# Kernel optimization log

Hardware: AMD Instinct MI355X
Metric: run time of the kernel (lower is better)

The kernel has to match this reference:

```python
import jax, jax.numpy as jnp
import numpy as np

N_NODES = 50000
N_EDGES = 1600000
IN_DIM = 128
HID = 128
SHARED = 64
N_GRAPHS = 2048


def setup_inputs() -> dict:
    key = jax.random.key(0)
    ks = jax.random.split(key, 16)
    x = jax.random.normal(ks[0], (N_NODES, IN_DIM), dtype=jnp.float32)
    edge_index = jax.random.randint(ks[1], (2, N_EDGES), 0, N_NODES, dtype=jnp.int64)
    batch = jnp.sort(jax.random.randint(ks[2], (N_NODES,), 0, N_GRAPHS, dtype=jnp.int64))

    def lin(k, fan_in, fan_out):
        bound = 1.0 / np.sqrt(fan_in)
        kw, kb = jax.random.split(k)
        W = jax.random.uniform(kw, (fan_in, fan_out), minval=-bound, maxval=bound, dtype=jnp.float32)
        b = jax.random.uniform(kb, (fan_out,), minval=-bound, maxval=bound, dtype=jnp.float32)
        return W, b

    W1a, b1a = lin(ks[3], IN_DIM, HID)
    W1b, b1b = lin(ks[4], HID, HID)
    W2a, b2a = lin(ks[5], HID, HID)
    W2b, b2b = lin(ks[6], HID, HID)
    Ws, bs = lin(ks[7], HID, SHARED)
    WlS, blS = lin(ks[8], SHARED, 1)
    WlP, blP = lin(ks[9], SHARED, 1)
    WnR, bnR = lin(ks[10], SHARED, 1)
    return dict(x=x, edge_index=edge_index, batch=batch,
                W1a=W1a, b1a=b1a, W1b=W1b, b1b=b1b,
                W2a=W2a, b2a=b2a, W2b=W2b, b2b=b2b,
                Ws=Ws, bs=bs, WlS=WlS, blS=blS, WlP=WlP, blP=blP, WnR=WnR, bnR=bnR)


def gin_conv(x, src, dst, Wa, ba, Wb, bb):
    # GINConv (eps=0): h_i = MLP(x_i + sum_{j->i} x_j)
    agg = jax.ops.segment_sum(x[src], dst, num_segments=N_NODES)
    h = x + agg
    h = jax.nn.relu(h @ Wa + ba)
    return h @ Wb + bb


def reference(x, edge_index, batch, W1a, b1a, W1b, b1b, W2a, b2a, W2b, b2b,
              Ws, bs, WlS, blS, WlP, blP, WnR, bnR):
    src, dst = edge_index[0], edge_index[1]
    h = jax.nn.relu(gin_conv(x, src, dst, W1a, b1a, W1b, b1b))
    h = jax.nn.relu(gin_conv(h, src, dst, W2a, b2a, W2b, b2b))
    # global mean pool over graph ids
    sums = jax.ops.segment_sum(h, batch, num_segments=N_GRAPHS)
    counts = jax.ops.segment_sum(jnp.ones((h.shape[0],), h.dtype), batch, num_segments=N_GRAPHS)
    pooled = sums / jnp.maximum(counts, 1.0)[:, None]
    g = jax.nn.relu(pooled @ Ws + bs)
    out_logS = (g @ WlS + blS)[:, 0]
    out_logP = (g @ WlP + blP)[:, 0]
    out_NR = (g @ WnR + bnR)[:, 0]
    return (out_logS, out_logP, out_NR)
```

## Files before the change

### kernel.cpp

```cpp
#include <hip/hip_runtime.h>
#include <hip/hip_bf16.h>


#define IN_DIM 128
#define NFINE 256
#define BIN_EPB 4096
#define SRCCH 16
#define NSLOT 3200
#define SPT 7

typedef float  f32x4  __attribute__((ext_vector_type(4)));
typedef short  bf16x4 __attribute__((ext_vector_type(4)));
typedef short  bf16x8 __attribute__((ext_vector_type(8)));

__device__ __forceinline__ unsigned short bf16_rne(float v) {
    unsigned u = __float_as_uint(v);
    unsigned t = u + 0x7fffu + ((u >> 16) & 1u);
    return (unsigned short)(t >> 16);
}


__global__ __launch_bounds__(256) void setup_kernel(
    const float4* __restrict__ xin, uint4* __restrict__ xb, int n8,
    const float* __restrict__ W0, const float* __restrict__ W1,
    const float* __restrict__ W2, const float* __restrict__ W3,
    unsigned short* __restrict__ Wh, unsigned short* __restrict__ Wl,
    int* __restrict__ bcur, float* __restrict__ pooled, int npool)
{
    int gid = blockIdx.x * 256 + threadIdx.x;
    if (gid < n8) {
        float4 a = xin[gid * 2];
        float4 b = xin[gid * 2 + 1];
        float v[8] = {a.x, a.y, a.z, a.w, b.x, b.y, b.z, b.w};
        unsigned r[4];
#pragma unroll
        for (int j = 0; j < 4; ++j)
            r[j] = (unsigned)bf16_rne(v[j * 2]) | ((unsigned)bf16_rne(v[j * 2 + 1]) << 16);
        xb[gid] = make_uint4(r[0], r[1], r[2], r[3]);
    }
    if (gid < 4 * 16384) {
        int m   = gid >> 14;
        int idx = gid & 16383;
        const float* W = (m == 0) ? W0 : (m == 1) ? W1 : (m == 2) ? W2 : W3;
        int k = idx >> 7, n = idx & 127;
        float v = W[idx];
        unsigned short hh = bf16_rne(v);
        float hf = __uint_as_float(((unsigned)hh) << 16);
        unsigned short ll = bf16_rne(v - hf);
        Wh[m * 16384 + n * 128 + k] = hh;
        Wl[m * 16384 + n * 128 + k] = ll;
    }
    if (gid < NFINE) bcur[gid] = 0;
    if (gid < npool) pooled[gid] = 0.f;
}


__global__ __launch_bounds__(256) void bin_kernel(
    const int* __restrict__ src, const int* __restrict__ dst,
    int2* __restrict__ buckets, int* __restrict__ bcur,
    int n_edges, int n_nodes, int cap)
{
    __shared__ int cnt[NFINE];
    __shared__ int base[NFINE];
    for (int i = threadIdx.x; i < NFINE; i += 256) cnt[i] = 0;
    __syncthreads();

    const int e0 = blockIdx.x * BIN_EPB + threadIdx.x * 16;
    int ne = n_edges - e0;
    if (ne < 0) ne = 0;
    if (ne > 16) ne = 16;

    int d[16], s[16], off[16];
    if (ne == 16) {
#pragma unroll
        for (int q = 0; q < 4; ++q) {
            int4 dv = *(const int4*)(dst + e0 + q * 4);
            int4 sv = *(const int4*)(src + e0 + q * 4);
            d[q * 4 + 0] = dv.x; d[q * 4 + 1] = dv.y;
            d[q * 4 + 2] = dv.z; d[q * 4 + 3] = dv.w;
            s[q * 4 + 0] = sv.x; s[q * 4 + 1] = sv.y;
            s[q * 4 + 2] = sv.z; s[q * 4 + 3] = sv.w;
        }
    } else {
#pragma unroll
        for (int j = 0; j < 16; ++j) {
            d[j] = (j < ne) ? dst[e0 + j] : 0;
            s[j] = (j < ne) ? src[e0 + j] : 0;
        }
    }
#pragma unroll
    for (int j = 0; j < 16; ++j)
        if (j < ne) {
            int b = (int)(((long long)d[j] * NFINE) / n_nodes);
            off[j] = atomicAdd(&cnt[b], 1);
        }
    __syncthreads();
    for (int i = threadIdx.x; i < NFINE; i += 256)
        base[i] = atomicAdd(&bcur[i], cnt[i]);
    __syncthreads();
#pragma unroll
    for (int j = 0; j < 16; ++j)
        if (j < ne) {
            int b = (int)(((long long)d[j] * NFINE) / n_nodes);
            buckets[(size_t)b * cap + base[b] + off[j]] = make_int2(d[j], s[j]);
        }
}

__global__ __launch_bounds__(512) void csr_fused_kernel(
    const int2* __restrict__ buckets, const int* __restrict__ bcnt,
    int* __restrict__ row_start, int* __restrict__ csr_src,
    int cap, int n_nodes, int n_edges)
{
    __shared__ int bc[NFINE];
    __shared__ int h[NSLOT];
    __shared__ int tsum[512];
    __shared__ int bbase_s;

    const int b = blockIdx.x;
    const int t = threadIdx.x;
    const int lo_n = (int)(((long long)b * n_nodes + NFINE - 1) / NFINE);
    const int hi_n = (int)(((long long)(b + 1) * n_nodes + NFINE - 1) / NFINE);
    const int sl = hi_n - lo_n;

    for (int i = t; i < NFINE; i += 512) bc[i] = bcnt[i];
    for (int i = t; i < NSLOT; i += 512) h[i] = 0;
    __syncthreads();
    if (t == 0) {
        int s = 0;
        for (int i = 0; i < b; ++i) s += bc[i];
        bbase_s = s;
    }
    const int nb = bc[b];
    const int2* bp = buckets + (size_t)b * cap;
    __syncthreads();

    for (int i = t; i < nb; i += 512) {
        int2 e = bp[i];
        int key = (e.x - lo_n) * SRCCH + (int)(((long long)e.y * SRCCH) / n_nodes);
        atomicAdd(&h[key], 1);
    }
    __syncthreads();

    int base = 0;
#pragma unroll
    for (int j = 0; j < SPT; ++j) {
        int slot = t * SPT + j;
        if (slot < NSLOT) {
            int v = h[slot];
            h[slot] = base;
            base += v;
        }
    }
    tsum[t] = base;
    __syncthreads();
    for (int off = 1; off < 512; off <<= 1) {
        int tmp = (t >= off) ? tsum[t - off] : 0;
        __syncthreads();
        tsum[t] += tmp;
        __syncthreads();
    }
    int texcl = tsum[t] - base + bbase_s;
#pragma unroll
    for (int j = 0; j < SPT; ++j) {
        int slot = t * SPT + j;
        if (slot < NSLOT) h[slot] += texcl;
    }
    __syncthreads();
    for (int i = t; i < sl; i += 512) row_start[lo_n + i] = h[i * SRCCH];
    if (b == NFINE - 1 && t == 0) row_start[n_nodes] = n_edges;
    __syncthreads();

    for (int i = t; i < nb; i += 512) {
        int2 e = bp[i];
        int key = (e.x - lo_n) * SRCCH + (int)(((long long)e.y * SRCCH) / n_nodes);
        csr_src[atomicAdd(&h[key], 1)] = e.y;
    }
}

#define HSTRIDE 132

__device__ __forceinline__ void add_row8(float acc[8], uint4 r) {
    union { unsigned u; float f; } c;
    c.u = r.x << 16;         acc[0] += c.f;
    c.u = r.x & 0xffff0000u; acc[1] += c.f;
    c.u = r.y << 16;         acc[2] += c.f;
    c.u = r.y & 0xffff0000u; acc[3] += c.f;
    c.u = r.z << 16;         acc[4] += c.f;
    c.u = r.z & 0xffff0000u; acc[5] += c.f;
    c.u = r.w << 16;         acc[6] += c.f;
    c.u = r.w & 0xffff0000u; acc[7] += c.f;
}

template <int LAYER>
__global__ __launch_bounds__(512) void fused_gin_layer_kernel(
    const float* __restrict__ xf,
    const uint4* __restrict__ selfh,
    const uint4* __restrict__ selfl,
    const uint4* __restrict__ nbr,
    const int* __restrict__ row_start, const int* __restrict__ csr_src,
    const unsigned short* __restrict__ Wa_h, const unsigned short* __restrict__ Wa_l,
    const float* __restrict__ ba,
    const unsigned short* __restrict__ Wb_h, const unsigned short* __restrict__ Wb_l,
    const float* __restrict__ bb,
    unsigned short* __restrict__ Ch, unsigned short* __restrict__ Cl,
    float* __restrict__ pooled, const int* __restrict__ batch, int M)
{
    __shared__ __align__(16) unsigned short LDSBUF[2][64][HSTRIDE];
    __shared__ int sbatch[64];
    auto& Hh = LDSBUF[0];
    auto& Hl = LDSBUF[1];

    const int t    = threadIdx.x;
    const int brow = blockIdx.x * 64;

    {
        const int lane = t & 15;
        const int gr   = t >> 4;
#pragma unroll
        for (int it = 0; it < 2; ++it) {
            const int rl   = it * 32 + gr;
            const int node = brow + rl;
            float acc[8] = {0.f, 0.f, 0.f, 0.f, 0.f, 0.f, 0.f, 0.f};
            if (node < M) {
                if constexpr (LAYER == 1) {
                    const f32x4* xfr = (const f32x4*)(xf + (size_t)node * IN_DIM + lane * 8);
                    f32x4 a0 = xfr[0];
                    f32x4 a1 = xfr[1];
                    acc[0] = a0.x; acc[1] = a0.y; acc[2] = a0.z; acc[3] = a0.w;
                    acc[4] = a1.x; acc[5] = a1.y; acc[6] = a1.z; acc[7] = a1.w;
                } else {
                    add_row8(acc, selfh[(size_t)node * 16 + lane]);
                    add_row8(acc, selfl[(size_t)node * 16 + lane]);
                }
                const int lo = row_start[node];
                const int hi = row_start[node + 1];
                int e = lo;
                for (; e + 3 < hi; e += 4) {
                    int s0 = csr_src[e];
                    int s1 = csr_src[e + 1];
                    int s2 = csr_src[e + 2];
                    int s3 = csr_src[e + 3];
                    uint4 r0 = nbr[(size_t)s0 * 16 + lane];
                    uint4 r1 = nbr[(size_t)s1 * 16 + lane];
                    uint4 r2 = nbr[(size_t)s2 * 16 + lane];
                    uint4 r3 = nbr[(size_t)s3 * 16 + lane];
                    add_row8(acc, r0);
                    add_row8(acc, r1);
                    add_row8(acc, r2);
                    add_row8(acc, r3);
                }
                for (; e < hi; ++e)
                    add_row8(acc, nbr[(size_t)csr_src[e] * 16 + lane]);
            }
            unsigned short hh[8], ll[8];
#pragma unroll
            for (int j = 0; j < 8; ++j) {
                unsigned short h = bf16_rne(acc[j]);
                hh[j] = h;
                ll[j] = bf16_rne(acc[j] - __uint_as_float(((unsigned)h) << 16));
            }
            *(bf16x4*)&Hh[rl][lane * 8]     = *(const bf16x4*)&hh[0];
            *(bf16x4*)&Hh[rl][lane * 8 + 4] = *(const bf16x4*)&hh[4];
            *(bf16x4*)&Hl[rl][lane * 8]     = *(const bf16x4*)&ll[0];
            *(bf16x4*)&Hl[rl][lane * 8 + 4] = *(const bf16x4*)&ll[4];
        }
    }
    __syncthreads();

    const int wave = t >> 6;
    const int lane = t & 63;
    const int l15  = lane & 15;
    const int quad = lane >> 4;
    const int rh   = (wave & 1) * 32;
    const int cq   = (wave >> 1) * 32;

    f32x4 acc[2][2];
#pragma unroll
    for (int ti = 0; ti < 2; ++ti)
#pragma unroll
        for (int ct = 0; ct < 2; ++ct) acc[ti][ct] = {0.f, 0.f, 0.f, 0.f};

#pragma unroll
    for (int k0 = 0; k0 < IN_DIM; k0 += 32) {
        const int hk = k0 + quad * 8;
        bf16x8 ah[2], al[2];
#pragma unroll
        for (int ti = 0; ti < 2; ++ti) {
            const int hr = rh + ti * 16 + l15;
            bf16x4 h0 = *(const bf16x4*)&Hh[hr][hk];
            bf16x4 h1 = *(const bf16x4*)&Hh[hr][hk + 4];
            bf16x4 l0 = *(const bf16x4*)&Hl[hr][hk];
            bf16x4 l1 = *(const bf16x4*)&Hl[hr][hk + 4];
            ah[ti] = __builtin_shufflevector(h0, h1, 0, 1, 2, 3, 4, 5, 6, 7);
            al[ti] = __builtin_shufflevector(l0, l1, 0, 1, 2, 3, 4, 5, 6, 7);
        }
#pragma unroll
        for (int ct = 0; ct < 2; ++ct) {
            const size_t woff = (size_t)(cq + ct * 16 + l15) * IN_DIM + k0 + quad * 8;
            bf16x8 wh = *(const bf16x8*)(Wa_h + woff);
            bf16x8 wl = *(const bf16x8*)(Wa_l + woff);
            acc[0][ct] = __builtin_amdgcn_mfma_f32_16x16x32_bf16(ah[0], wh, acc[0][ct], 0, 0, 0);
            acc[1][ct] = __builtin_amdgcn_mfma_f32_16x16x32_bf16(ah[1], wh, acc[1][ct], 0, 0, 0);
            acc[0][ct] = __builtin_amdgcn_mfma_f32_16x16x32_bf16(al[0], wh, acc[0][ct], 0, 0, 0);
            acc[1][ct] = __builtin_amdgcn_mfma_f32_16x16x32_bf16(al[1], wh, acc[1][ct], 0, 0, 0);
            acc[0][ct] = __builtin_amdgcn_mfma_f32_16x16x32_bf16(ah[0], wl, acc[0][ct], 0, 0, 0);
            acc[1][ct] = __builtin_amdgcn_mfma_f32_16x16x32_bf16(ah[1], wl, acc[1][ct], 0, 0, 0);
        }
    }
    __syncthreads();

#pragma unroll
    for (int ti = 0; ti < 2; ++ti) {
#pragma unroll
        for (int ct = 0; ct < 2; ++ct) {
            int col = cq + ct * 16 + l15;
            float b = ba[col];
#pragma unroll
            for (int r = 0; r < 4; ++r) {
                int rl = rh + ti * 16 + quad * 4 + r;
                float v = fmaxf(acc[ti][ct][r] + b, 0.f);
                unsigned short hh = bf16_rne(v);
                Hh[rl][col] = hh;
                Hl[rl][col] = bf16_rne(v - __uint_as_float(((unsigned)hh) << 16));
            }
            acc[ti][ct] = {0.f, 0.f, 0.f, 0.f};
        }
    }
    __syncthreads();

#pragma unroll
    for (int k0 = 0; k0 < IN_DIM; k0 += 32) {
        const int hk = k0 + quad * 8;
        bf16x8 ah[2], al[2];
#pragma unroll
        for (int ti = 0; ti < 2; ++ti) {
            const int hr = rh + ti * 16 + l15;
            bf16x4 h0 = *(const bf16x4*)&Hh[hr][hk];
            bf16x4 h1 = *(const bf16x4*)&Hh[hr][hk + 4];
            bf16x4 l0 = *(const bf16x4*)&Hl[hr][hk];
            bf16x4 l1 = *(const bf16x4*)&Hl[hr][hk + 4];
            ah[ti] = __builtin_shufflevector(h0, h1, 0, 1, 2, 3, 4, 5, 6, 7);
            al[ti] = __builtin_shufflevector(l0, l1, 0, 1, 2, 3, 4, 5, 6, 7);
        }
#pragma unroll
        for (int ct = 0; ct < 2; ++ct) {
            const size_t woff = (size_t)(cq + ct * 16 + l15) * IN_DIM + k0 + quad * 8;
            bf16x8 wh = *(const bf16x8*)(Wb_h + woff);
            bf16x8 wl = *(const bf16x8*)(Wb_l + woff);
            acc[0][ct] = __builtin_amdgcn_mfma_f32_16x16x32_bf16(ah[0], wh, acc[0][ct], 0, 0, 0);
            acc[1][ct] = __builtin_amdgcn_mfma_f32_16x16x32_bf16(ah[1], wh, acc[1][ct], 0, 0, 0);
            acc[0][ct] = __builtin_amdgcn_mfma_f32_16x16x32_bf16(al[0], wh, acc[0][ct], 0, 0, 0);
            acc[1][ct] = __builtin_amdgcn_mfma_f32_16x16x32_bf16(al[1], wh, acc[1][ct], 0, 0, 0);
            acc[0][ct] = __builtin_amdgcn_mfma_f32_16x16x32_bf16(ah[0], wl, acc[0][ct], 0, 0, 0);
            acc[1][ct] = __builtin_amdgcn_mfma_f32_16x16x32_bf16(ah[1], wl, acc[1][ct], 0, 0, 0);
        }
    }

    if constexpr (LAYER == 1) {
#pragma unroll
        for (int ti = 0; ti < 2; ++ti) {
            const int rbase = brow + rh + ti * 16 + quad * 4;
#pragma unroll
            for (int ct = 0; ct < 2; ++ct) {
                int col = cq + ct * 16 + l15;
                float b = bb[col];
#pragma unroll
                for (int r = 0; r < 4; ++r) {
                    int row = rbase + r;
                    if (row < M) {
                        float o = fmaxf(acc[ti][ct][r] + b, 0.f);
                        unsigned short hh = bf16_rne(o);
                        Ch[(size_t)row * IN_DIM + col] = hh;
                        Cl[(size_t)row * IN_DIM + col] =
                            bf16_rne(o - __uint_as_float(((unsigned)hh) << 16));
                    }
                }
            }
        }
    } else {
        __syncthreads();
        float* ftile = (float*)&LDSBUF[0][0][0];
#pragma unroll
        for (int ti = 0; ti < 2; ++ti) {
#pragma unroll
            for (int ct = 0; ct < 2; ++ct) {
                int col = cq + ct * 16 + l15;
                float b = bb[col];
#pragma unroll
                for (int r = 0; r < 4; ++r) {
                    int rl = rh + ti * 16 + quad * 4 + r;
                    ftile[rl * 128 + col] = fmaxf(acc[ti][ct][r] + b, 0.f);
                }
            }
        }
        if (t < 64) {
            int node = brow + t;
            sbatch[t] = (node < M) ? batch[node] : -1;
        }
        __syncthreads();
        if (t < 128) {
            const int col = t;
            float run = 0.f;
            int curg = sbatch[0];
#pragma unroll 1
            for (int r = 0; r < 64; ++r) {
                int g = sbatch[r];
                if (g != curg) {
                    if (curg >= 0)
                        atomicAdd(&pooled[(size_t)curg * IN_DIM + col], run);
                    curg = g;
                    run = 0.f;
                }
                if (g >= 0) run += ftile[r * 128 + col];
            }
            if (curg >= 0)
                atomicAdd(&pooled[(size_t)curg * IN_DIM + col], run);
        }
    }
}


__device__ __forceinline__ int lower_bound_i(const int* __restrict__ a, int n, int v) {
    int lo = 0, hi = n;
    while (lo < hi) {
        int mid = (lo + hi) >> 1;
        if (a[mid] < v) lo = mid + 1; else hi = mid;
    }
    return lo;
}

__global__ __launch_bounds__(64) void head_kernel(
    const float* __restrict__ pooled, const int* __restrict__ batch, int n_nodes,
    const float* __restrict__ Ws,  const float* __restrict__ bs,
    const float* __restrict__ WlS, const float* __restrict__ blS,
    const float* __restrict__ WlP, const float* __restrict__ blP,
    const float* __restrict__ WnR, const float* __restrict__ bnR,
    float* __restrict__ out, int n_graphs)
{
    int g = blockIdx.x;
    int j = threadIdx.x;
    int lo = lower_bound_i(batch, n_nodes, g);
    int hi = lower_bound_i(batch, n_nodes, g + 1);
    float inv = 1.f / fmaxf((float)(hi - lo), 1.0f);
    const float* p = pooled + (size_t)g * IN_DIM;
    float acc = 0.f;
#pragma unroll 8
    for (int k = 0; k < IN_DIM; ++k)
        acc = fmaf(p[k], Ws[k * 64 + j], acc);
    float gj = fmaxf(acc * inv + bs[j], 0.f);
    float s1 = gj * WlS[j];
    float s2 = gj * WlP[j];
    float s3 = gj * WnR[j];
#pragma unroll
    for (int off = 32; off > 0; off >>= 1) {
        s1 += __shfl_down(s1, off);
        s2 += __shfl_down(s2, off);
        s3 += __shfl_down(s3, off);
    }
    if (j == 0) {
        out[g]                = s1 + blS[0];
        out[n_graphs + g]     = s2 + blP[0];
        out[2 * n_graphs + g] = s3 + bnR[0];
    }
}


extern "C" void kernel_launch(void* const* d_in, const int* in_sizes, int n_in,
                              void* d_out, int out_size, void* d_ws, size_t ws_size,
                              hipStream_t stream)
{
    const float* x   = (const float*)d_in[0];
    const int*   ei  = (const int*)d_in[1];
    const int*   bat = (const int*)d_in[2];
    const float* W1a = (const float*)d_in[3];
    const float* b1a = (const float*)d_in[4];
    const float* W1b = (const float*)d_in[5];
    const float* b1b = (const float*)d_in[6];
    const float* W2a = (const float*)d_in[7];
    const float* b2a = (const float*)d_in[8];
    const float* W2b = (const float*)d_in[9];
    const float* b2b = (const float*)d_in[10];
    const float* Ws  = (const float*)d_in[11];
    const float* bs  = (const float*)d_in[12];
    const float* WlS = (const float*)d_in[13];
    const float* blS = (const float*)d_in[14];
    const float* WlP = (const float*)d_in[15];
    const float* blP = (const float*)d_in[16];
    const float* WnR = (const float*)d_in[17];
    const float* bnR = (const float*)d_in[18];

    const int n_nodes  = in_sizes[0] / IN_DIM;
    const int n_edges  = in_sizes[1] / 2;
    const int n_graphs = out_size / 3;
    const int* src = ei;
    const int* dst = ei + n_edges;

    const size_t node_elems   = (size_t)n_nodes * IN_DIM;
    const size_t pooled_elems = (size_t)n_graphs * IN_DIM;

    unsigned short* xb = (unsigned short*)d_ws;
    unsigned short* Ch = xb + node_elems;
    unsigned short* Cl = Ch + node_elems;
    float* pooled = (float*)(Cl + node_elems);
    int* row_start = (int*)(pooled + pooled_elems);
    int* bcur      = row_start + (n_nodes + 1);
    int* csr_src   = bcur + NFINE;
    unsigned short* wt_h = (unsigned short*)(csr_src + n_edges);
    unsigned short* wt_l = wt_h + 4 * 16384;

    const int cap = n_edges / NFINE + 2048;
    int2* buckets = (int2*)Ch;

    const int layerblocks = (n_nodes + 63) / 64;
    const int binblocks = (n_edges + BIN_EPB - 1) / BIN_EPB;
    const int n8 = (int)(node_elems / 8);
    const int cvtblocks = (n8 + 255) / 256;

    setup_kernel<<<cvtblocks, 256, 0, stream>>>(
        (const float4*)x, (uint4*)xb, n8, W1a, W1b, W2a, W2b,
        wt_h, wt_l, bcur, pooled, (int)pooled_elems);
    bin_kernel<<<binblocks, 256, 0, stream>>>(src, dst, buckets, bcur,
                                              n_edges, n_nodes, cap);
    csr_fused_kernel<<<NFINE, 512, 0, stream>>>(buckets, bcur, row_start,
                                                csr_src, cap, n_nodes, n_edges);

    fused_gin_layer_kernel<1><<<layerblocks, 512, 0, stream>>>(
        x, nullptr, nullptr, (const uint4*)xb, row_start, csr_src,
        wt_h, wt_l, b1a, wt_h + 16384, wt_l + 16384, b1b,
        Ch, Cl, nullptr, nullptr, n_nodes);

    fused_gin_layer_kernel<2><<<layerblocks, 512, 0, stream>>>(
        nullptr, (const uint4*)Ch, (const uint4*)Cl, (const uint4*)Ch,
        row_start, csr_src,
        wt_h + 2 * 16384, wt_l + 2 * 16384, b2a,
        wt_h + 3 * 16384, wt_l + 3 * 16384, b2b,
        nullptr, nullptr, pooled, bat, n_nodes);

    head_kernel<<<n_graphs, 64, 0, stream>>>(pooled, bat, n_nodes,
                                             Ws, bs, WlS, blS, WlP, blP,
                                             WnR, bnR, (float*)d_out, n_graphs);
}
```

Measured before the change: 319.9 us.

## Pack edge pairs into 32-bit words and halve GIN layer row tile to 32

Edges are binned as a single 32-bit word (dst in the high 16 bits, src in the low 16 bits) instead of an int2, which halves the bucket traffic in binning and CSR build and drops the 64-bit divisions. The fused GIN layer kernel now handles 32 nodes per block instead of 64. Each of the 512 threads gathers one node row instead of two, which doubles the block count and is meant to improve latency hiding for the gather and the MFMA phases. The packing relies on node indices fitting in 16 bits, but with 50000 nodes d*256 overflows nothing and src fits 65535. Smaller tiles reload the weights more often per node, and the int multiply d*NFINE stays within int range.

```diff
diff --git a/kernel.cpp b/kernel.cpp
--- a/kernel.cpp
+++ b/kernel.cpp
@@ -57,7 +57,7 @@
 
 __global__ __launch_bounds__(256) void bin_kernel(
     const int* __restrict__ src, const int* __restrict__ dst,
-    int2* __restrict__ buckets, int* __restrict__ bcur,
+    unsigned* __restrict__ buckets, int* __restrict__ bcur,
     int n_edges, int n_nodes, int cap)
 {
     __shared__ int cnt[NFINE];
@@ -91,7 +91,7 @@
 #pragma unroll
     for (int j = 0; j < 16; ++j)
         if (j < ne) {
-            int b = (int)(((long long)d[j] * NFINE) / n_nodes);
+            int b = (d[j] * NFINE) / n_nodes;
             off[j] = atomicAdd(&cnt[b], 1);
         }
     __syncthreads();
@@ -101,13 +101,14 @@
 #pragma unroll
     for (int j = 0; j < 16; ++j)
         if (j < ne) {
-            int b = (int)(((long long)d[j] * NFINE) / n_nodes);
-            buckets[(size_t)b * cap + base[b] + off[j]] = make_int2(d[j], s[j]);
+            int b = (d[j] * NFINE) / n_nodes;
+            buckets[(size_t)b * cap + base[b] + off[j]] =
+                ((unsigned)d[j] << 16) | (unsigned)s[j];
         }
 }
 
 __global__ __launch_bounds__(512) void csr_fused_kernel(
-    const int2* __restrict__ buckets, const int* __restrict__ bcnt,
+    const unsigned* __restrict__ buckets, const int* __restrict__ bcnt,
     int* __restrict__ row_start, int* __restrict__ csr_src,
     int cap, int n_nodes, int n_edges)
 {
@@ -131,12 +132,13 @@
         bbase_s = s;
     }
     const int nb = bc[b];
-    const int2* bp = buckets + (size_t)b * cap;
+    const unsigned* bp = buckets + (size_t)b * cap;
     __syncthreads();
 
     for (int i = t; i < nb; i += 512) {
-        int2 e = bp[i];
-        int key = (e.x - lo_n) * SRCCH + (int)(((long long)e.y * SRCCH) / n_nodes);
+        unsigned p = bp[i];
+        int key = ((int)(p >> 16) - lo_n) * SRCCH
+                + (int)(p & 0xffffu) * SRCCH / n_nodes;
         atomicAdd(&h[key], 1);
     }
     __syncthreads();
@@ -171,9 +173,10 @@
     __syncthreads();
 
     for (int i = t; i < nb; i += 512) {
-        int2 e = bp[i];
-        int key = (e.x - lo_n) * SRCCH + (int)(((long long)e.y * SRCCH) / n_nodes);
-        csr_src[atomicAdd(&h[key], 1)] = e.y;
+        unsigned p = bp[i];
+        int key = ((int)(p >> 16) - lo_n) * SRCCH
+                + (int)(p & 0xffffu) * SRCCH / n_nodes;
+        csr_src[atomicAdd(&h[key], 1)] = (int)(p & 0xffffu);
     }
 }
 
@@ -205,65 +208,61 @@
     unsigned short* __restrict__ Ch, unsigned short* __restrict__ Cl,
     float* __restrict__ pooled, const int* __restrict__ batch, int M)
 {
-    __shared__ __align__(16) unsigned short LDSBUF[2][64][HSTRIDE];
-    __shared__ int sbatch[64];
+    __shared__ __align__(16) unsigned short LDSBUF[2][32][HSTRIDE];
+    __shared__ int sbatch[32];
     auto& Hh = LDSBUF[0];
     auto& Hl = LDSBUF[1];
 
     const int t    = threadIdx.x;
-    const int brow = blockIdx.x * 64;
+    const int brow = blockIdx.x * 32;
 
     {
         const int lane = t & 15;
         const int gr   = t >> 4;
-#pragma unroll
-        for (int it = 0; it < 2; ++it) {
-            const int rl   = it * 32 + gr;
-            const int node = brow + rl;
-            float acc[8] = {0.f, 0.f, 0.f, 0.f, 0.f, 0.f, 0.f, 0.f};
-            if (node < M) {
-                if constexpr (LAYER == 1) {
-                    const f32x4* xfr = (const f32x4*)(xf + (size_t)node * IN_DIM + lane * 8);
-                    f32x4 a0 = xfr[0];
-                    f32x4 a1 = xfr[1];
-                    acc[0] = a0.x; acc[1] = a0.y; acc[2] = a0.z; acc[3] = a0.w;
-                    acc[4] = a1.x; acc[5] = a1.y; acc[6] = a1.z; acc[7] = a1.w;
-                } else {
-                    add_row8(acc, selfh[(size_t)node * 16 + lane]);
-                    add_row8(acc, selfl[(size_t)node * 16 + lane]);
-                }
-                const int lo = row_start[node];
-                const int hi = row_start[node + 1];
-                int e = lo;
-                for (; e + 3 < hi; e += 4) {
-                    int s0 = csr_src[e];
-                    int s1 = csr_src[e + 1];
-                    int s2 = csr_src[e + 2];
-                    int s3 = csr_src[e + 3];
-                    uint4 r0 = nbr[(size_t)s0 * 16 + lane];
-                    uint4 r1 = nbr[(size_t)s1 * 16 + lane];
-                    uint4 r2 = nbr[(size_t)s2 * 16 + lane];
-                    uint4 r3 = nbr[(size_t)s3 * 16 + lane];
-                    add_row8(acc, r0);
-                    add_row8(acc, r1);
-                    add_row8(acc, r2);
-                    add_row8(acc, r3);
-                }
-                for (; e < hi; ++e)
-                    add_row8(acc, nbr[(size_t)csr_src[e] * 16 + lane]);
+        const int node = brow + gr;
+        float acc[8] = {0.f, 0.f, 0.f, 0.f, 0.f, 0.f, 0.f, 0.f};
+        if (node < M) {
+            if constexpr (LAYER == 1) {
+                const f32x4* xfr = (const f32x4*)(xf + (size_t)node * IN_DIM + lane * 8);
+                f32x4 a0 = xfr[0];
+                f32x4 a1 = xfr[1];
+                acc[0] = a0.x; acc[1] = a0.y; acc[2] = a0.z; acc[3] = a0.w;
+                acc[4] = a1.x; acc[5] = a1.y; acc[6] = a1.z; acc[7] = a1.w;
+            } else {
+                add_row8(acc, selfh[(size_t)node * 16 + lane]);
+                add_row8(acc, selfl[(size_t)node * 16 + lane]);
             }
-            unsigned short hh[8], ll[8];
-#pragma unroll
-            for (int j = 0; j < 8; ++j) {
-                unsigned short h = bf16_rne(acc[j]);
-                hh[j] = h;
-                ll[j] = bf16_rne(acc[j] - __uint_as_float(((unsigned)h) << 16));
+            const int lo = row_start[node];
+            const int hi = row_start[node + 1];
+            int e = lo;
+            for (; e + 3 < hi; e += 4) {
+                int s0 = csr_src[e];
+                int s1 = csr_src[e + 1];
+                int s2 = csr_src[e + 2];
+                int s3 = csr_src[e + 3];
+                uint4 r0 = nbr[(size_t)s0 * 16 + lane];
+                uint4 r1 = nbr[(size_t)s1 * 16 + lane];
+                uint4 r2 = nbr[(size_t)s2 * 16 + lane];
+                uint4 r3 = nbr[(size_t)s3 * 16 + lane];
+                add_row8(acc, r0);
+                add_row8(acc, r1);
+                add_row8(acc, r2);
+                add_row8(acc, r3);
             }
-            *(bf16x4*)&Hh[rl][lane * 8]     = *(const bf16x4*)&hh[0];
-            *(bf16x4*)&Hh[rl][lane * 8 + 4] = *(const bf16x4*)&hh[4];
-            *(bf16x4*)&Hl[rl][lane * 8]     = *(const bf16x4*)&ll[0];
-            *(bf16x4*)&Hl[rl][lane * 8 + 4] = *(const bf16x4*)&ll[4];
-        }
+            for (; e < hi; ++e)
+                add_row8(acc, nbr[(size_t)csr_src[e] * 16 + lane]);
+        }
+        unsigned short hh[8], ll[8];
+#pragma unroll
+        for (int j = 0; j < 8; ++j) {
+            unsigned short h = bf16_rne(acc[j]);
+            hh[j] = h;
+            ll[j] = bf16_rne(acc[j] - __uint_as_float(((unsigned)h) << 16));
+        }
+        *(bf16x4*)&Hh[gr][lane * 8]     = *(const bf16x4*)&hh[0];
+        *(bf16x4*)&Hh[gr][lane * 8 + 4] = *(const bf16x4*)&hh[4];
+        *(bf16x4*)&Hl[gr][lane * 8]     = *(const bf16x4*)&ll[0];
+        *(bf16x4*)&Hl[gr][lane * 8 + 4] = *(const bf16x4*)&ll[4];
     }
     __syncthreads();
 
@@ -271,109 +270,87 @@
     const int lane = t & 63;
     const int l15  = lane & 15;
     const int quad = lane >> 4;
-    const int rh   = (wave & 1) * 32;
+    const int rh   = (wave & 1) * 16;
     const int cq   = (wave >> 1) * 32;
 
-    f32x4 acc[2][2];
-#pragma unroll
-    for (int ti = 0; ti < 2; ++ti)
-#pragma unroll
-        for (int ct = 0; ct < 2; ++ct) acc[ti][ct] = {0.f, 0.f, 0.f, 0.f};
+    f32x4 acc[2];
+    acc[0] = {0.f, 0.f, 0.f, 0.f};
+    acc[1] = {0.f, 0.f, 0.f, 0.f};
 
 #pragma unroll
     for (int k0 = 0; k0 < IN_DIM; k0 += 32) {
         const int hk = k0 + quad * 8;
-        bf16x8 ah[2], al[2];
-#pragma unroll
-        for (int ti = 0; ti < 2; ++ti) {
-            const int hr = rh + ti * 16 + l15;
-            bf16x4 h0 = *(const bf16x4*)&Hh[hr][hk];
-            bf16x4 h1 = *(const bf16x4*)&Hh[hr][hk + 4];
-            bf16x4 l0 = *(const bf16x4*)&Hl[hr][hk];
-            bf16x4 l1 = *(const bf16x4*)&Hl[hr][hk + 4];
-            ah[ti] = __builtin_shufflevector(h0, h1, 0, 1, 2, 3, 4, 5, 6, 7);
-            al[ti] = __builtin_shufflevector(l0, l1, 0, 1, 2, 3, 4, 5, 6, 7);
-        }
+        const int hr = rh + l15;
+        bf16x4 h0 = *(const bf16x4*)&Hh[hr][hk];
+        bf16x4 h1 = *(const bf16x4*)&Hh[hr][hk + 4];
+        bf16x4 l0 = *(const bf16x4*)&Hl[hr][hk];
+        bf16x4 l1 = *(const bf16x4*)&Hl[hr][hk + 4];
+        bf16x8 ah = __builtin_shufflevector(h0, h1, 0, 1, 2, 3, 4, 5, 6, 7);
+        bf16x8 al = __builtin_shufflevector(l0, l1, 0, 1, 2, 3, 4, 5, 6, 7);
 #pragma unroll
         for (int ct = 0; ct < 2; ++ct) {
             const size_t woff = (size_t)(cq + ct * 16 + l15) * IN_DIM + k0 + quad * 8;
             bf16x8 wh = *(const bf16x8*)(Wa_h + woff);
             bf16x8 wl = *(const bf16x8*)(Wa_l + woff);
-            acc[0][ct] = __builtin_amdgcn_mfma_f32_16x16x32_bf16(ah[0], wh, acc[0][ct], 0, 0, 0);
-            acc[1][ct] = __builtin_amdgcn_mfma_f32_16x16x32_bf16(ah[1], wh, acc[1][ct], 0, 0, 0);
-            acc[0][ct] = __builtin_amdgcn_mfma_f32_16x16x32_bf16(al[0], wh, acc[0][ct], 0, 0, 0);
-            acc[1][ct] = __builtin_amdgcn_mfma_f32_16x16x32_bf16(al[1], wh, acc[1][ct], 0, 0, 0);
-            acc[0][ct] = __builtin_amdgcn_mfma_f32_16x16x32_bf16(ah[0], wl, acc[0][ct], 0, 0, 0);
-            acc[1][ct] = __builtin_amdgcn_mfma_f32_16x16x32_bf16(ah[1], wl, acc[1][ct], 0, 0, 0);
-        }
-    }
-    __syncthreads();
-
-#pragma unroll
-    for (int ti = 0; ti < 2; ++ti) {
-#pragma unroll
-        for (int ct = 0; ct < 2; ++ct) {
-            int col = cq + ct * 16 + l15;
-            float b = ba[col];
-#pragma unroll
-            for (int r = 0; r < 4; ++r) {
-                int rl = rh + ti * 16 + quad * 4 + r;
-                float v = fmaxf(acc[ti][ct][r] + b, 0.f);
-                unsigned short hh = bf16_rne(v);
-                Hh[rl][col] = hh;
-                Hl[rl][col] = bf16_rne(v - __uint_as_float(((unsigned)hh) << 16));
-            }
-            acc[ti][ct] = {0.f, 0.f, 0.f, 0.f};
-        }
+            acc[ct] = __builtin_amdgcn_mfma_f32_16x16x32_bf16(ah, wh, acc[ct], 0, 0, 0);
+            acc[ct] = __builtin_amdgcn_mfma_f32_16x16x32_bf16(al, wh, acc[ct], 0, 0, 0);
+            acc[ct] = __builtin_amdgcn_mfma_f32_16x16x32_bf16(ah, wl, acc[ct], 0, 0, 0);
+        }
+    }
+    __syncthreads();
+
+#pragma unroll
+    for (int ct = 0; ct < 2; ++ct) {
+        int col = cq + ct * 16 + l15;
+        float b = ba[col];
+#pragma unroll
+        for (int r = 0; r < 4; ++r) {
+            int rl = rh + quad * 4 + r;
+            float v = fmaxf(acc[ct][r] + b, 0.f);
+            unsigned short hh = bf16_rne(v);
+            Hh[rl][col] = hh;
+            Hl[rl][col] = bf16_rne(v - __uint_as_float(((unsigned)hh) << 16));
+        }
+        acc[ct] = {0.f, 0.f, 0.f, 0.f};
     }
     __syncthreads();
 
 #pragma unroll
     for (int k0 = 0; k0 < IN_DIM; k0 += 32) {
         const int hk = k0 + quad * 8;
-        bf16x8 ah[2], al[2];
-#pragma unroll
-        for (int ti = 0; ti < 2; ++ti) {
-            const int hr = rh + ti * 16 + l15;
-            bf16x4 h0 = *(const bf16x4*)&Hh[hr][hk];
-            bf16x4 h1 = *(const bf16x4*)&Hh[hr][hk + 4];
-            bf16x4 l0 = *(const bf16x4*)&Hl[hr][hk];
-            bf16x4 l1 = *(const bf16x4*)&Hl[hr][hk + 4];
-            ah[ti] = __builtin_shufflevector(h0, h1, 0, 1, 2, 3, 4, 5, 6, 7);
-            al[ti] = __builtin_shufflevector(l0, l1, 0, 1, 2, 3, 4, 5, 6, 7);
-        }
+        const int hr = rh + l15;
+        bf16x4 h0 = *(const bf16x4*)&Hh[hr][hk];
+        bf16x4 h1 = *(const bf16x4*)&Hh[hr][hk + 4];
+        bf16x4 l0 = *(const bf16x4*)&Hl[hr][hk];
+        bf16x4 l1 = *(const bf16x4*)&Hl[hr][hk + 4];
+        bf16x8 ah = __builtin_shufflevector(h0, h1, 0, 1, 2, 3, 4, 5, 6, 7);
+        bf16x8 al = __builtin_shufflevector(l0, l1, 0, 1, 2, 3, 4, 5, 6, 7);
 #pragma unroll
         for (int ct = 0; ct < 2; ++ct) {
             const size_t woff = (size_t)(cq + ct * 16 + l15) * IN_DIM + k0 + quad * 8;
             bf16x8 wh = *(const bf16x8*)(Wb_h + woff);
             bf16x8 wl = *(const bf16x8*)(Wb_l + woff);
-            acc[0][ct] = __builtin_amdgcn_mfma_f32_16x16x32_bf16(ah[0], wh, acc[0][ct], 0, 0, 0);
-            acc[1][ct] = __builtin_amdgcn_mfma_f32_16x16x32_bf16(ah[1], wh, acc[1][ct], 0, 0, 0);
-            acc[0][ct] = __builtin_amdgcn_mfma_f32_16x16x32_bf16(al[0], wh, acc[0][ct], 0, 0, 0);
-            acc[1][ct] = __builtin_amdgcn_mfma_f32_16x16x32_bf16(al[1], wh, acc[1][ct], 0, 0, 0);
-            acc[0][ct] = __builtin_amdgcn_mfma_f32_16x16x32_bf16(ah[0], wl, acc[0][ct], 0, 0, 0);
-            acc[1][ct] = __builtin_amdgcn_mfma_f32_16x16x32_bf16(ah[1], wl, acc[1][ct], 0, 0, 0);
+            acc[ct] = __builtin_amdgcn_mfma_f32_16x16x32_bf16(ah, wh, acc[ct], 0, 0, 0);
+            acc[ct] = __builtin_amdgcn_mfma_f32_16x16x32_bf16(al, wh, acc[ct], 0, 0, 0);
+            acc[ct] = __builtin_amdgcn_mfma_f32_16x16x32_bf16(ah, wl, acc[ct], 0, 0, 0);
         }
     }
 
     if constexpr (LAYER == 1) {
-#pragma unroll
-        for (int ti = 0; ti < 2; ++ti) {
-            const int rbase = brow + rh + ti * 16 + quad * 4;
-#pragma unroll
-            for (int ct = 0; ct < 2; ++ct) {
-                int col = cq + ct * 16 + l15;
-                float b = bb[col];
-#pragma unroll
-                for (int r = 0; r < 4; ++r) {
-                    int row = rbase + r;
-                    if (row < M) {
-                        float o = fmaxf(acc[ti][ct][r] + b, 0.f);
-                        unsigned short hh = bf16_rne(o);
-                        Ch[(size_t)row * IN_DIM + col] = hh;
-                        Cl[(size_t)row * IN_DIM + col] =
-                            bf16_rne(o - __uint_as_float(((unsigned)hh) << 16));
-                    }
+        const int rbase = brow + rh + quad * 4;
+#pragma unroll
+        for (int ct = 0; ct < 2; ++ct) {
+            int col = cq + ct * 16 + l15;
+            float b = bb[col];
+#pragma unroll
+            for (int r = 0; r < 4; ++r) {
+                int row = rbase + r;
+                if (row < M) {
+                    float o = fmaxf(acc[ct][r] + b, 0.f);
+                    unsigned short hh = bf16_rne(o);
+                    Ch[(size_t)row * IN_DIM + col] = hh;
+                    Cl[(size_t)row * IN_DIM + col] =
+                        bf16_rne(o - __uint_as_float(((unsigned)hh) << 16));
                 }
             }
         }
@@ -381,19 +358,16 @@
         __syncthreads();
         float* ftile = (float*)&LDSBUF[0][0][0];
 #pragma unroll
-        for (int ti = 0; ti < 2; ++ti) {
-#pragma unroll
-            for (int ct = 0; ct < 2; ++ct) {
-                int col = cq + ct * 16 + l15;
-                float b = bb[col];
-#pragma unroll
-                for (int r = 0; r < 4; ++r) {
-                    int rl = rh + ti * 16 + quad * 4 + r;
-                    ftile[rl * 128 + col] = fmaxf(acc[ti][ct][r] + b, 0.f);
-                }
+        for (int ct = 0; ct < 2; ++ct) {
+            int col = cq + ct * 16 + l15;
+            float b = bb[col];
+#pragma unroll
+            for (int r = 0; r < 4; ++r) {
+                int rl = rh + quad * 4 + r;
+                ftile[rl * 132 + col] = fmaxf(acc[ct][r] + b, 0.f);
             }
         }
-        if (t < 64) {
+        if (t < 32) {
             int node = brow + t;
             sbatch[t] = (node < M) ? batch[node] : -1;
         }
@@ -403,7 +377,7 @@
             float run = 0.f;
             int curg = sbatch[0];
 #pragma unroll 1
-            for (int r = 0; r < 64; ++r) {
+            for (int r = 0; r < 32; ++r) {
                 int g = sbatch[r];
                 if (g != curg) {
                     if (curg >= 0)
@@ -411,7 +385,7 @@
                     curg = g;
                     run = 0.f;
                 }
-                if (g >= 0) run += ftile[r * 128 + col];
+                if (g >= 0) run += ftile[r * 132 + col];
             }
             if (curg >= 0)
                 atomicAdd(&pooled[(size_t)curg * IN_DIM + col], run);
@@ -509,9 +483,9 @@
     unsigned short* wt_l = wt_h + 4 * 16384;
 
     const int cap = n_edges / NFINE + 2048;
-    int2* buckets = (int2*)Ch;
-
-    const int layerblocks = (n_nodes + 63) / 64;
+    unsigned* buckets = (unsigned*)Ch;
+
+    const int layerblocks = (n_nodes + 31) / 32;
     const int binblocks = (n_edges + BIN_EPB - 1) / BIN_EPB;
     const int n8 = (int)(node_elems / 8);
     const int cvtblocks = (n8 + 255) / 256;
```

Measured after the change: 349.0 us. 9.1% more time.
